# Kernel tuning notes

Hardware: AMD Instinct MI355X
Metric: run time of the kernel (lower is better)

Reference implementation:

```python
import jax, jax.numpy as jnp
import numpy as np

B, S, E = 8, 4096, 128
H, O = 64, 64  # attention_hidden_dim, out_dim


def setup_inputs() -> dict:
    key = jax.random.key(0)
    ks = jax.random.split(key, 4)
    x = jax.random.normal(ks[0], (B, S, E), dtype=jnp.float32)
    Wq = jax.random.normal(ks[1], (E, H), dtype=jnp.float32) * (1.0 / np.sqrt(E))
    Wk = jax.random.normal(ks[2], (E, H), dtype=jnp.float32) * (1.0 / np.sqrt(E))
    Wv = jax.random.normal(ks[3], (E, O), dtype=jnp.float32) * (1.0 / np.sqrt(E))
    bq = jnp.zeros((H,), dtype=jnp.float32)
    bk = jnp.zeros((H,), dtype=jnp.float32)
    bv = jnp.zeros((O,), dtype=jnp.float32)
    return {"x": x, "Wq": Wq, "bq": bq, "Wk": Wk, "bk": bk, "Wv": Wv, "bv": bv}


def reference(x, Wq, bq, Wk, bk, Wv, bv):
    # Batched version of the per-sample loop: q = x@Wq+bq, etc.
    q = jnp.einsum("bse,eh->bsh", x, Wq) + bq   # [B,S,H]
    k = jnp.einsum("bse,eh->bsh", x, Wk) + bk   # [B,S,H]
    v = jnp.einsum("bse,eo->bso", x, Wv) + bv   # [B,S,O]
    scores = jnp.einsum("bqh,bkh->bqk", q, k)   # QK^T per sample, [B,S,S]
    attn = jax.nn.softmax(scores, axis=-1)       # softmax over key dim
    out = jnp.einsum("bqk,bko->bqo", attn, v)   # [B,S,O]
    return out
```

## Files before the change

### kernel.cpp

```cpp
#include <hip/hip_runtime.h>
#include <math.h>

#define BB 8
#define SS 4096
#define EE 128
#define HH 64

typedef _Float16 f16;
typedef __attribute__((ext_vector_type(8))) _Float16 f16x8;
typedef __attribute__((ext_vector_type(4))) float f32x4;

__device__ __forceinline__ unsigned short f2h(float v) {
    f16 h = (f16)v;
    return __builtin_bit_cast(unsigned short, h);
}

__global__ __launch_bounds__(256) void wtrans_kernel(
    const float* __restrict__ Wq, const float* __restrict__ Wk,
    const float* __restrict__ Wv, f16* __restrict__ Wt)
{
    const int idx = blockIdx.x * 256 + threadIdx.x;
    if (idx >= 192 * 128) return;
    const int col = idx >> 7, e = idx & 127;
    const float v = (col < 64)  ? Wq[e * 64 + col]
                  : (col < 128) ? Wk[e * 64 + (col - 64)]
                                : Wv[e * 64 + (col - 128)];
    Wt[col * 128 + e] = (f16)v;
}

__global__ __launch_bounds__(256) void qkv_kernel(
    const float* __restrict__ x, const f16* __restrict__ Wt,
    const float* __restrict__ bq, const float* __restrict__ bk,
    const float* __restrict__ bv,
    f16* __restrict__ Q, f16* __restrict__ K, f16* __restrict__ Vt)
{
    __shared__ __align__(16) short xs[64 * EE];
    const int tid = threadIdx.x;
    const long rowbase = (long)blockIdx.x * 64;

    {
        const float4* xg = (const float4*)(x + rowbase * EE);
#pragma unroll
        for (int j = 0; j < 8; ++j) {
            const int eidx = tid * 32 + j * 4;
            const float4 v = xg[eidx >> 2];
            unsigned long long pk =
                (unsigned long long)f2h(v.x) |
                ((unsigned long long)f2h(v.y) << 16) |
                ((unsigned long long)f2h(v.z) << 32) |
                ((unsigned long long)f2h(v.w) << 48);
            const int row = eidx >> 7;
            const int off = (row * 256 + (eidx & 127) * 2) ^ ((row & 7) << 4);
            *(unsigned long long*)((char*)xs + off) = pk;
        }
    }
    __syncthreads();

    const int lane = tid & 63;
    const int wid  = tid >> 6;
    const int ln15 = lane & 15;
    const int lg   = lane >> 4;

    f16x8 xa[4];
    {
        const int row = wid * 16 + ln15;
        const int swz = (row & 7) << 4;
#pragma unroll
        for (int s = 0; s < 4; ++s) {
            const int off = (row * 256 + lg * 16 + s * 64) ^ swz;
            xa[s] = *(const f16x8*)((const char*)xs + off);
        }
    }

    f32x4 acc[12];
#pragma unroll
    for (int ct = 0; ct < 12; ++ct) acc[ct] = (f32x4){0.f, 0.f, 0.f, 0.f};

#pragma unroll
    for (int ct = 0; ct < 12; ++ct) {
        const f16* wtp = Wt + (ct * 16 + ln15) * 128 + lg * 8;
#pragma unroll
        for (int s = 0; s < 4; ++s) {
            const f16x8 wb = *(const f16x8*)(wtp + s * 32);
            acc[ct] = __builtin_amdgcn_mfma_f32_16x16x32_f16(xa[s], wb, acc[ct], 0, 0, 0);
        }
    }

    const long grow0 = rowbase + wid * 16 + 4 * lg;
#pragma unroll
    for (int ct = 0; ct < 4; ++ct) {
        const int col = ct * 16 + ln15;
        const float b = bq[col];
#pragma unroll
        for (int r = 0; r < 4; ++r)
            Q[(grow0 + r) * HH + col] = (f16)(acc[ct][r] + b);
    }
#pragma unroll
    for (int ct = 4; ct < 8; ++ct) {
        const int col = (ct - 4) * 16 + ln15;
        const float b = bk[col];
#pragma unroll
        for (int r = 0; r < 4; ++r)
            K[(grow0 + r) * HH + col] = (f16)(acc[ct][r] + b);
    }
    {
        const long batch = rowbase >> 12;
        const long inrow = (rowbase & 4095) + wid * 16 + 4 * lg;
#pragma unroll
        for (int ct = 8; ct < 12; ++ct) {
            const int o = (ct - 8) * 16 + ln15;
            const float b = bv[o];
            unsigned long long pk =
                (unsigned long long)f2h(acc[ct][0] + b) |
                ((unsigned long long)f2h(acc[ct][1] + b) << 16) |
                ((unsigned long long)f2h(acc[ct][2] + b) << 32) |
                ((unsigned long long)f2h(acc[ct][3] + b) << 48);
            *(unsigned long long*)(Vt + ((long)batch * HH + o) * SS + inrow) = pk;
        }
    }
}

__global__ __launch_bounds__(256, 4) void flash_kernel(
    const f16* __restrict__ Q, const f16* __restrict__ K,
    const f16* __restrict__ Vt, float* __restrict__ Opart,
    float* __restrict__ ml)
{
    __shared__ __align__(16) short k_s[64 * HH];
    __shared__ __align__(16) short v_s[64 * HH];
    __shared__ __align__(16) short p_s[4 * 16 * HH];

    const int tid  = threadIdx.x;
    const int lane = tid & 63;
    const int wid  = tid >> 6;
    const int ln15 = lane & 15;
    const int lg   = lane >> 4;
    const int batch = blockIdx.x & 7;
    const int rest  = blockIdx.x >> 3;
    const int split = rest & 1;
    const int qtile = rest >> 1;
    const int k0base = split * (SS / 2);

    f16x8 qf[2];
    {
        const long qrow = (long)batch * SS + qtile * 64 + wid * 16 + ln15;
        const f16* qp = Q + qrow * HH + lg * 8;
        qf[0] = *(const f16x8*)(qp);
        qf[1] = *(const f16x8*)(qp + 32);
    }

    f32x4 oacc[4];
#pragma unroll
    for (int ot = 0; ot < 4; ++ot) oacc[ot] = (f32x4){0.f, 0.f, 0.f, 0.f};
    float m = -1e30f, l = 0.f;

    short* pw = p_s + wid * (16 * HH);
    const int swq = (ln15 & 7) << 4;

    const int srow = tid >> 3;
    const int scc  = tid & 7;
    const int d0 = (srow * 128 + scc * 16) ^ ((srow & 7) << 4);
    const int d1 = ((srow + 32) * 128 + scc * 16) ^ (((srow + 32) & 7) << 4);

    uint4 kr0, kr1, vr0, vr1;
    {
        const uint4* kb = (const uint4*)(K + ((long)batch * SS + k0base) * HH);
        kr0 = kb[tid]; kr1 = kb[tid + 256];
        const f16* vb = Vt + (long)batch * HH * SS + k0base;
        vr0 = *(const uint4*)(vb + (long)srow * SS + scc * 8);
        vr1 = *(const uint4*)(vb + (long)(srow + 32) * SS + scc * 8);
        *(uint4*)((char*)k_s + d0) = kr0;
        *(uint4*)((char*)k_s + d1) = kr1;
        *(uint4*)((char*)v_s + d0) = vr0;
        *(uint4*)((char*)v_s + d1) = vr1;
    }
    __syncthreads();

    for (int t = 0; t < 32; ++t) {
        if (t + 1 < 32) {
            const int k0 = k0base + (t + 1) * 64;
            const uint4* kb = (const uint4*)(K + ((long)batch * SS + k0) * HH);
            kr0 = kb[tid]; kr1 = kb[tid + 256];
            const f16* vb = Vt + (long)batch * HH * SS + k0;
            vr0 = *(const uint4*)(vb + (long)srow * SS + scc * 8);
            vr1 = *(const uint4*)(vb + (long)(srow + 32) * SS + scc * 8);
        }

        f32x4 sacc[4];
#pragma unroll
        for (int kt = 0; kt < 4; ++kt) {
            f32x4 a = (f32x4){0.f, 0.f, 0.f, 0.f};
            const int key = kt * 16 + ln15;
            const int rb = key * 128, swz = (key & 7) << 4;
#pragma unroll
            for (int s = 0; s < 2; ++s) {
                const f16x8 ka = *(const f16x8*)((const char*)k_s + ((rb + lg * 16 + s * 64) ^ swz));
                a = __builtin_amdgcn_mfma_f32_16x16x32_f16(ka, qf[s], a, 0, 0, 0);
            }
            sacc[kt] = a;
        }

        float tm = sacc[0][0];
#pragma unroll
        for (int kt = 0; kt < 4; ++kt)
#pragma unroll
            for (int r = 0; r < 4; ++r) tm = fmaxf(tm, sacc[kt][r]);
        tm = fmaxf(tm, __shfl_xor(tm, 16));
        tm = fmaxf(tm, __shfl_xor(tm, 32));
        if (!__all(tm <= m + 8.0f)) {
            const float mn = fmaxf(m, tm);
            const float alpha = __expf(m - mn);
            l *= alpha;
#pragma unroll
            for (int r = 0; r < 4; ++r) {
                const float ar = __shfl(alpha, lg * 4 + r);
                oacc[0][r] *= ar; oacc[1][r] *= ar;
                oacc[2][r] *= ar; oacc[3][r] *= ar;
            }
            m = mn;
        }

        float p[16];
#pragma unroll
        for (int kt = 0; kt < 4; ++kt)
#pragma unroll
            for (int r = 0; r < 4; ++r)
                p[kt * 4 + r] = __expf(sacc[kt][r] - m);
        float ps = 0.f;
#pragma unroll
        for (int j = 0; j < 16; ++j) ps += p[j];
        ps += __shfl_xor(ps, 16);
        ps += __shfl_xor(ps, 32);
        l += ps;

#pragma unroll
        for (int kt = 0; kt < 4; ++kt)
#pragma unroll
            for (int rp = 0; rp < 2; ++rp) {
                const unsigned int pk =
                    (unsigned int)f2h(p[kt * 4 + 2 * rp]) |
                    ((unsigned int)f2h(p[kt * 4 + 2 * rp + 1]) << 16);
                const int key = kt * 16 + lg * 4 + rp * 2;
                *(unsigned int*)((char*)pw + ((ln15 * 128 + key * 2) ^ swq)) = pk;
            }

#pragma unroll
        for (int s = 0; s < 2; ++s) {
            const f16x8 pa = *(const f16x8*)((const char*)pw + ((ln15 * 128 + lg * 16 + s * 64) ^ swq));
#pragma unroll
            for (int ot = 0; ot < 4; ++ot) {
                const int o = ot * 16 + ln15;
                const f16x8 vb = *(const f16x8*)((const char*)v_s + ((o * 128 + lg * 16 + s * 64) ^ ((o & 7) << 4)));
                oacc[ot] = __builtin_amdgcn_mfma_f32_16x16x32_f16(pa, vb, oacc[ot], 0, 0, 0);
            }
        }

        __syncthreads();
        if (t + 1 < 32) {
            *(uint4*)((char*)k_s + d0) = kr0;
            *(uint4*)((char*)k_s + d1) = kr1;
            *(uint4*)((char*)v_s + d0) = vr0;
            *(uint4*)((char*)v_s + d1) = vr1;
        }
        __syncthreads();
    }

    const long ridx = (long)batch * SS + qtile * 64 + wid * 16;
#pragma unroll
    for (int r = 0; r < 4; ++r) {
        float* op = Opart + ((long)split * (BB * SS) + ridx + lg * 4 + r) * HH + ln15;
        op[0]  = oacc[0][r];
        op[16] = oacc[1][r];
        op[32] = oacc[2][r];
        op[48] = oacc[3][r];
    }
    if (lg == 0) {
        float* mlp = ml + ((long)split * (BB * SS) + ridx + ln15) * 2;
        mlp[0] = m;
        mlp[1] = l;
    }
}

__global__ __launch_bounds__(256) void merge_kernel(
    const float* __restrict__ Opart, const float* __restrict__ ml,
    float* __restrict__ Out)
{
    const int gid = blockIdx.x * 256 + threadIdx.x;
    const long row = gid >> 2;
    const int c0 = (gid & 3) * 16;
    const float m0 = ml[row * 2], l0 = ml[row * 2 + 1];
    const float m1 = ml[(BB * SS + row) * 2], l1 = ml[(BB * SS + row) * 2 + 1];
    const float M = fmaxf(m0, m1);
    const float w0 = __expf(m0 - M), w1 = __expf(m1 - M);
    const float inv = 1.0f / (w0 * l0 + w1 * l1);
    const float4* o0 = (const float4*)(Opart + row * HH + c0);
    const float4* o1 = (const float4*)(Opart + ((long)BB * SS + row) * HH + c0);
    float4* dst = (float4*)(Out + row * HH + c0);
#pragma unroll
    for (int i = 0; i < 4; ++i) {
        const float4 a = o0[i], b = o1[i];
        float4 r;
        r.x = (w0 * a.x + w1 * b.x) * inv;
        r.y = (w0 * a.y + w1 * b.y) * inv;
        r.z = (w0 * a.z + w1 * b.z) * inv;
        r.w = (w0 * a.w + w1 * b.w) * inv;
        dst[i] = r;
    }
}

extern "C" void kernel_launch(void* const* d_in, const int* in_sizes, int n_in,
                              void* d_out, int out_size, void* d_ws, size_t ws_size,
                              hipStream_t stream) {
    const float* x  = (const float*)d_in[0];
    const float* Wq = (const float*)d_in[1];
    const float* bq = (const float*)d_in[2];
    const float* Wk = (const float*)d_in[3];
    const float* bk = (const float*)d_in[4];
    const float* Wv = (const float*)d_in[5];
    const float* bv = (const float*)d_in[6];
    float* out = (float*)d_out;

    const size_t NTOK = (size_t)BB * SS;
    f16* Q  = (f16*)d_ws;
    f16* K  = Q + NTOK * HH;
    f16* Vt = K + NTOK * HH;
    f16* Wt = Vt + NTOK * HH;
    float* Opart = (float*)(Wt + 192 * 128);
    float* ml = Opart + 2 * NTOK * HH;

    wtrans_kernel<<<96, 256, 0, stream>>>(Wq, Wk, Wv, Wt);
    qkv_kernel<<<BB * SS / 64, 256, 0, stream>>>(x, Wt, bq, bk, bv, Q, K, Vt);
    flash_kernel<<<BB * 2 * (SS / 64), 256, 0, stream>>>(Q, K, Vt, Opart, ml);
    merge_kernel<<<BB * SS * 4 / 256, 256, 0, stream>>>(Opart, ml, out);
}
```

Before: 93.59 us.

## Rework flash attention into a 4-way KV split with 512-thread blocks and exp2 softmax

The flash kernel now uses 512-thread blocks covering 128 queries and a 4-way split of the key range instead of 2-way. Each thread loads one K and one V vector per tile instead of two. Log2(e) is folded into Wq and bq so the softmax can use exp2, the rescale threshold is raised, and MFMA sections get s_setprio hints. Partial outputs are stored normalized in fp16 together with an LSE value, which cuts merge traffic but doubles the number of partials to combine and lowers the precision of the intermediates. Conversions use packed cvt_pkrtz, which rounds toward zero rather than to nearest.

```diff
diff --git a/kernel.cpp b/kernel.cpp
--- a/kernel.cpp
+++ b/kernel.cpp
@@ -5,14 +5,19 @@
 #define SS 4096
 #define EE 128
 #define HH 64
+#define LOG2E 1.44269504088896f
 
 typedef _Float16 f16;
 typedef __attribute__((ext_vector_type(8))) _Float16 f16x8;
+typedef __attribute__((ext_vector_type(2))) _Float16 f16x2;
 typedef __attribute__((ext_vector_type(4))) float f32x4;
 
 __device__ __forceinline__ unsigned short f2h(float v) {
     f16 h = (f16)v;
     return __builtin_bit_cast(unsigned short, h);
+}
+__device__ __forceinline__ unsigned int pk2h(float a, float b) {
+    return __builtin_bit_cast(unsigned int, __builtin_amdgcn_cvt_pkrtz(a, b));
 }
 
 __global__ __launch_bounds__(256) void wtrans_kernel(
@@ -22,7 +27,7 @@
     const int idx = blockIdx.x * 256 + threadIdx.x;
     if (idx >= 192 * 128) return;
     const int col = idx >> 7, e = idx & 127;
-    const float v = (col < 64)  ? Wq[e * 64 + col]
+    const float v = (col < 64)  ? Wq[e * 64 + col] * LOG2E
                   : (col < 128) ? Wk[e * 64 + (col - 64)]
                                 : Wv[e * 64 + (col - 128)];
     Wt[col * 128 + e] = (f16)v;
@@ -45,10 +50,8 @@
             const int eidx = tid * 32 + j * 4;
             const float4 v = xg[eidx >> 2];
             unsigned long long pk =
-                (unsigned long long)f2h(v.x) |
-                ((unsigned long long)f2h(v.y) << 16) |
-                ((unsigned long long)f2h(v.z) << 32) |
-                ((unsigned long long)f2h(v.w) << 48);
+                (unsigned long long)pk2h(v.x, v.y) |
+                ((unsigned long long)pk2h(v.z, v.w) << 32);
             const int row = eidx >> 7;
             const int off = (row * 256 + (eidx & 127) * 2) ^ ((row & 7) << 4);
             *(unsigned long long*)((char*)xs + off) = pk;
@@ -66,10 +69,8 @@
         const int row = wid * 16 + ln15;
         const int swz = (row & 7) << 4;
 #pragma unroll
-        for (int s = 0; s < 4; ++s) {
-            const int off = (row * 256 + lg * 16 + s * 64) ^ swz;
-            xa[s] = *(const f16x8*)((const char*)xs + off);
-        }
+        for (int s = 0; s < 4; ++s)
+            xa[s] = *(const f16x8*)((const char*)xs + ((row * 256 + lg * 16 + s * 64) ^ swz));
     }
 
     f32x4 acc[12];
@@ -90,7 +91,7 @@
 #pragma unroll
     for (int ct = 0; ct < 4; ++ct) {
         const int col = ct * 16 + ln15;
-        const float b = bq[col];
+        const float b = bq[col] * LOG2E;
 #pragma unroll
         for (int r = 0; r < 4; ++r)
             Q[(grow0 + r) * HH + col] = (f16)(acc[ct][r] + b);
@@ -111,23 +112,21 @@
             const int o = (ct - 8) * 16 + ln15;
             const float b = bv[o];
             unsigned long long pk =
-                (unsigned long long)f2h(acc[ct][0] + b) |
-                ((unsigned long long)f2h(acc[ct][1] + b) << 16) |
-                ((unsigned long long)f2h(acc[ct][2] + b) << 32) |
-                ((unsigned long long)f2h(acc[ct][3] + b) << 48);
+                (unsigned long long)pk2h(acc[ct][0] + b, acc[ct][1] + b) |
+                ((unsigned long long)pk2h(acc[ct][2] + b, acc[ct][3] + b) << 32);
             *(unsigned long long*)(Vt + ((long)batch * HH + o) * SS + inrow) = pk;
         }
     }
 }
 
-__global__ __launch_bounds__(256, 4) void flash_kernel(
+__global__ __launch_bounds__(512, 8) void flash_kernel(
     const f16* __restrict__ Q, const f16* __restrict__ K,
-    const f16* __restrict__ Vt, float* __restrict__ Opart,
-    float* __restrict__ ml)
+    const f16* __restrict__ Vt, f16* __restrict__ Onorm,
+    float* __restrict__ lse)
 {
     __shared__ __align__(16) short k_s[64 * HH];
     __shared__ __align__(16) short v_s[64 * HH];
-    __shared__ __align__(16) short p_s[4 * 16 * HH];
+    __shared__ __align__(16) short p_s[8 * 16 * HH];
 
     const int tid  = threadIdx.x;
     const int lane = tid & 63;
@@ -136,13 +135,13 @@
     const int lg   = lane >> 4;
     const int batch = blockIdx.x & 7;
     const int rest  = blockIdx.x >> 3;
-    const int split = rest & 1;
-    const int qtile = rest >> 1;
-    const int k0base = split * (SS / 2);
+    const int split = rest & 3;
+    const int qblk  = rest >> 2;
+    const int k0base = split * (SS / 4);
 
     f16x8 qf[2];
     {
-        const long qrow = (long)batch * SS + qtile * 64 + wid * 16 + ln15;
+        const long qrow = (long)batch * SS + qblk * 128 + wid * 16 + ln15;
         const f16* qp = Q + qrow * HH + lg * 8;
         qf[0] = *(const f16x8*)(qp);
         qf[1] = *(const f16x8*)(qp + 32);
@@ -159,33 +158,25 @@
     const int srow = tid >> 3;
     const int scc  = tid & 7;
     const int d0 = (srow * 128 + scc * 16) ^ ((srow & 7) << 4);
-    const int d1 = ((srow + 32) * 128 + scc * 16) ^ (((srow + 32) & 7) << 4);
-
-    uint4 kr0, kr1, vr0, vr1;
-    {
-        const uint4* kb = (const uint4*)(K + ((long)batch * SS + k0base) * HH);
-        kr0 = kb[tid]; kr1 = kb[tid + 256];
-        const f16* vb = Vt + (long)batch * HH * SS + k0base;
-        vr0 = *(const uint4*)(vb + (long)srow * SS + scc * 8);
-        vr1 = *(const uint4*)(vb + (long)(srow + 32) * SS + scc * 8);
-        *(uint4*)((char*)k_s + d0) = kr0;
-        *(uint4*)((char*)k_s + d1) = kr1;
-        *(uint4*)((char*)v_s + d0) = vr0;
-        *(uint4*)((char*)v_s + d1) = vr1;
-    }
+
+    const uint4* kb = (const uint4*)(K + ((long)batch * SS + k0base) * HH);
+    const f16* vbase = Vt + (long)batch * HH * SS + k0base;
+
+    uint4 kr, vr;
+    kr = kb[tid];
+    vr = *(const uint4*)(vbase + (long)srow * SS + scc * 8);
+    *(uint4*)((char*)k_s + d0) = kr;
+    *(uint4*)((char*)v_s + d0) = vr;
     __syncthreads();
 
-    for (int t = 0; t < 32; ++t) {
-        if (t + 1 < 32) {
-            const int k0 = k0base + (t + 1) * 64;
-            const uint4* kb = (const uint4*)(K + ((long)batch * SS + k0) * HH);
-            kr0 = kb[tid]; kr1 = kb[tid + 256];
-            const f16* vb = Vt + (long)batch * HH * SS + k0;
-            vr0 = *(const uint4*)(vb + (long)srow * SS + scc * 8);
-            vr1 = *(const uint4*)(vb + (long)(srow + 32) * SS + scc * 8);
+    for (int t = 0; t < 16; ++t) {
+        if (t + 1 < 16) {
+            kr = kb[tid + (t + 1) * 512];
+            vr = *(const uint4*)(vbase + (t + 1) * 64 + (long)srow * SS + scc * 8);
         }
 
         f32x4 sacc[4];
+        __builtin_amdgcn_s_setprio(1);
 #pragma unroll
         for (int kt = 0; kt < 4; ++kt) {
             f32x4 a = (f32x4){0.f, 0.f, 0.f, 0.f};
@@ -198,17 +189,19 @@
             }
             sacc[kt] = a;
         }
-
-        float tm = sacc[0][0];
-#pragma unroll
-        for (int kt = 0; kt < 4; ++kt)
-#pragma unroll
-            for (int r = 0; r < 4; ++r) tm = fmaxf(tm, sacc[kt][r]);
+        __builtin_amdgcn_s_setprio(0);
+
+        float t0 = fmaxf(fmaxf(sacc[0][0], sacc[0][1]), sacc[0][2]);
+        float t1 = fmaxf(fmaxf(sacc[0][3], sacc[1][0]), sacc[1][1]);
+        float t2 = fmaxf(fmaxf(sacc[1][2], sacc[1][3]), sacc[2][0]);
+        float t3 = fmaxf(fmaxf(sacc[2][1], sacc[2][2]), sacc[2][3]);
+        float t4 = fmaxf(fmaxf(sacc[3][0], sacc[3][1]), sacc[3][2]);
+        float tm = fmaxf(fmaxf(fmaxf(t0, t1), t2), fmaxf(fmaxf(t3, t4), sacc[3][3]));
         tm = fmaxf(tm, __shfl_xor(tm, 16));
         tm = fmaxf(tm, __shfl_xor(tm, 32));
-        if (!__all(tm <= m + 8.0f)) {
+        if (!__all(tm <= m + 11.5f)) {
             const float mn = fmaxf(m, tm);
-            const float alpha = __expf(m - mn);
+            const float alpha = __builtin_amdgcn_exp2f(m - mn);
             l *= alpha;
 #pragma unroll
             for (int r = 0; r < 4; ++r) {
@@ -219,30 +212,29 @@
             m = mn;
         }
 
-        float p[16];
+        float ps = 0.f;
 #pragma unroll
         for (int kt = 0; kt < 4; ++kt)
 #pragma unroll
-            for (int r = 0; r < 4; ++r)
-                p[kt * 4 + r] = __expf(sacc[kt][r] - m);
-        float ps = 0.f;
-#pragma unroll
-        for (int j = 0; j < 16; ++j) ps += p[j];
+            for (int r = 0; r < 4; ++r) {
+                const float pv = __builtin_amdgcn_exp2f(sacc[kt][r] - m);
+                sacc[kt][r] = pv;
+                ps += pv;
+            }
         ps += __shfl_xor(ps, 16);
         ps += __shfl_xor(ps, 32);
         l += ps;
 
 #pragma unroll
-        for (int kt = 0; kt < 4; ++kt)
-#pragma unroll
-            for (int rp = 0; rp < 2; ++rp) {
-                const unsigned int pk =
-                    (unsigned int)f2h(p[kt * 4 + 2 * rp]) |
-                    ((unsigned int)f2h(p[kt * 4 + 2 * rp + 1]) << 16);
-                const int key = kt * 16 + lg * 4 + rp * 2;
-                *(unsigned int*)((char*)pw + ((ln15 * 128 + key * 2) ^ swq)) = pk;
-            }
-
+        for (int kt = 0; kt < 4; ++kt) {
+            uint2 pk;
+            pk.x = pk2h(sacc[kt][0], sacc[kt][1]);
+            pk.y = pk2h(sacc[kt][2], sacc[kt][3]);
+            const int key = kt * 16 + lg * 4;
+            *(uint2*)((char*)pw + ((ln15 * 128 + key * 2) ^ swq)) = pk;
+        }
+
+        __builtin_amdgcn_s_setprio(1);
 #pragma unroll
         for (int s = 0; s < 2; ++s) {
             const f16x8 pa = *(const f16x8*)((const char*)pw + ((ln15 * 128 + lg * 16 + s * 64) ^ swq));
@@ -253,58 +245,64 @@
                 oacc[ot] = __builtin_amdgcn_mfma_f32_16x16x32_f16(pa, vb, oacc[ot], 0, 0, 0);
             }
         }
+        __builtin_amdgcn_s_setprio(0);
 
         __syncthreads();
-        if (t + 1 < 32) {
-            *(uint4*)((char*)k_s + d0) = kr0;
-            *(uint4*)((char*)k_s + d1) = kr1;
-            *(uint4*)((char*)v_s + d0) = vr0;
-            *(uint4*)((char*)v_s + d1) = vr1;
+        if (t + 1 < 16) {
+            *(uint4*)((char*)k_s + d0) = kr;
+            *(uint4*)((char*)v_s + d0) = vr;
         }
         __syncthreads();
     }
 
-    const long ridx = (long)batch * SS + qtile * 64 + wid * 16;
+    const float linv = 1.0f / l;
+    const long ridx = (long)split * (BB * SS) + (long)batch * SS + qblk * 128 + wid * 16;
 #pragma unroll
     for (int r = 0; r < 4; ++r) {
-        float* op = Opart + ((long)split * (BB * SS) + ridx + lg * 4 + r) * HH + ln15;
-        op[0]  = oacc[0][r];
-        op[16] = oacc[1][r];
-        op[32] = oacc[2][r];
-        op[48] = oacc[3][r];
-    }
-    if (lg == 0) {
-        float* mlp = ml + ((long)split * (BB * SS) + ridx + ln15) * 2;
-        mlp[0] = m;
-        mlp[1] = l;
-    }
+        const float ir = __shfl(linv, lg * 4 + r);
+        f16* op = Onorm + (ridx + lg * 4 + r) * HH + ln15;
+        op[0]  = (f16)(oacc[0][r] * ir);
+        op[16] = (f16)(oacc[1][r] * ir);
+        op[32] = (f16)(oacc[2][r] * ir);
+        op[48] = (f16)(oacc[3][r] * ir);
+    }
+    if (lg == 0)
+        lse[ridx + ln15] = m + __builtin_amdgcn_logf(l);
 }
 
 __global__ __launch_bounds__(256) void merge_kernel(
-    const float* __restrict__ Opart, const float* __restrict__ ml,
+    const f16* __restrict__ Onorm, const float* __restrict__ lse,
     float* __restrict__ Out)
 {
     const int gid = blockIdx.x * 256 + threadIdx.x;
-    const long row = gid >> 2;
-    const int c0 = (gid & 3) * 16;
-    const float m0 = ml[row * 2], l0 = ml[row * 2 + 1];
-    const float m1 = ml[(BB * SS + row) * 2], l1 = ml[(BB * SS + row) * 2 + 1];
-    const float M = fmaxf(m0, m1);
-    const float w0 = __expf(m0 - M), w1 = __expf(m1 - M);
-    const float inv = 1.0f / (w0 * l0 + w1 * l1);
-    const float4* o0 = (const float4*)(Opart + row * HH + c0);
-    const float4* o1 = (const float4*)(Opart + ((long)BB * SS + row) * HH + c0);
+    const long row = gid >> 3;
+    const int c0 = (gid & 7) * 8;
+    const long NR = (long)BB * SS;
+
+    float ls[4];
+#pragma unroll
+    for (int i = 0; i < 4; ++i) ls[i] = lse[i * NR + row];
+    const float M = fmaxf(fmaxf(ls[0], ls[1]), fmaxf(ls[2], ls[3]));
+    float g[4], denom = 0.f;
+#pragma unroll
+    for (int i = 0; i < 4; ++i) { g[i] = __builtin_amdgcn_exp2f(ls[i] - M); denom += g[i]; }
+    const float inv = 1.0f / denom;
+
+    float acc[8];
+#pragma unroll
+    for (int j = 0; j < 8; ++j) acc[j] = 0.f;
+#pragma unroll
+    for (int i = 0; i < 4; ++i) {
+        const f16x8 o = *(const f16x8*)(Onorm + (i * NR + row) * HH + c0);
+#pragma unroll
+        for (int j = 0; j < 8; ++j) acc[j] = fmaf(g[i], (float)o[j], acc[j]);
+    }
+    float4 r0, r1;
+    r0.x = acc[0] * inv; r0.y = acc[1] * inv; r0.z = acc[2] * inv; r0.w = acc[3] * inv;
+    r1.x = acc[4] * inv; r1.y = acc[5] * inv; r1.z = acc[6] * inv; r1.w = acc[7] * inv;
     float4* dst = (float4*)(Out + row * HH + c0);
-#pragma unroll
-    for (int i = 0; i < 4; ++i) {
-        const float4 a = o0[i], b = o1[i];
-        float4 r;
-        r.x = (w0 * a.x + w1 * b.x) * inv;
-        r.y = (w0 * a.y + w1 * b.y) * inv;
-        r.z = (w0 * a.z + w1 * b.z) * inv;
-        r.w = (w0 * a.w + w1 * b.w) * inv;
-        dst[i] = r;
-    }
+    dst[0] = r0;
+    dst[1] = r1;
 }
 
 extern "C" void kernel_launch(void* const* d_in, const int* in_sizes, int n_in,
@@ -324,11 +322,11 @@
     f16* K  = Q + NTOK * HH;
     f16* Vt = K + NTOK * HH;
     f16* Wt = Vt + NTOK * HH;
-    float* Opart = (float*)(Wt + 192 * 128);
-    float* ml = Opart + 2 * NTOK * HH;
+    f16* Onorm = Wt + 192 * 128;
+    float* lse = (float*)(Onorm + 4 * NTOK * HH);
 
     wtrans_kernel<<<96, 256, 0, stream>>>(Wq, Wk, Wv, Wt);
     qkv_kernel<<<BB * SS / 64, 256, 0, stream>>>(x, Wt, bq, bk, bv, Q, K, Vt);
-    flash_kernel<<<BB * 2 * (SS / 64), 256, 0, stream>>>(Q, K, Vt, Opart, ml);
-    merge_kernel<<<BB * SS * 4 / 256, 256, 0, stream>>>(Opart, ml, out);
-}
+    flash_kernel<<<BB * 4 * (SS / 128), 512, 0, stream>>>(Q, K, Vt, Onorm, lse);
+    merge_kernel<<<BB * SS * 8 / 256, 256, 0, stream>>>(Onorm, lse, out);
+}
```

Measured after the change: 125.9 us. 1.35x slower.
